# Optimization experiments

Measured on AMD Instinct MI355X. Metric: run time of the kernel, lower is better.

Reference implementation:

```python
import jax, jax.numpy as jnp
import numpy as np

B, H, E, R, T = 2048, 512, 300, 512, 50


def setup_inputs() -> dict:
    key = jax.random.key(0)
    ks = jax.random.split(key, 12)
    s = 0.02  # xavier-ish scale for params
    return {
        "x": jax.random.normal(ks[0], (B, E), jnp.float32),
        "h_enc": jax.random.normal(ks[1], (B, R), jnp.float32),
        "phi_history": jax.random.normal(ks[2], (T, B, H), jnp.float32),
        "cell_history": jax.random.normal(ks[3], (T, B, H), jnp.float32),
        "h_summ": jax.random.normal(ks[4], (B, H), jnp.float32),
        "c_summ": jax.random.normal(ks[5], (B, H), jnp.float32),
        "W_w": jax.random.normal(ks[6], (4 * H, H + E), jnp.float32) * s,
        "W_b": jnp.zeros((4 * H,), jnp.float32),
        "v_w": jax.random.normal(ks[7], (1, H), jnp.float32) * s,
        "v_b": jnp.zeros((1,), jnp.float32),
        "lq_w": jax.random.normal(ks[8], (H, R), jnp.float32) * s,
        "lq_b": jnp.zeros((H,), jnp.float32),
        "lk_w": jax.random.normal(ks[9], (H, H), jnp.float32) * s,
        "lk_b": jnp.zeros((H,), jnp.float32),
        "ls_w": jax.random.normal(ks[10], (H, H), jnp.float32) * s,
        "ls_b": jnp.zeros((H,), jnp.float32),
    }


def reference(x, h_enc, phi_history, cell_history, h_summ, c_summ,
              W_w, W_b, v_w, v_b, lq_w, lq_b, lk_w, lk_b, ls_w, ls_b):
    Hd = h_summ.shape[-1]
    # [T,B,H] -> [B,T,H] (torch.stack(...).transpose(0,1))
    phi = jnp.transpose(phi_history, (1, 0, 2))
    cell = jnp.transpose(cell_history, (1, 0, 2))
    # additive attention over cached history
    q = h_enc @ lq_w.T + lq_b                       # [B,H]
    k = jnp.einsum('bth,ah->bta', phi, lk_w) + lk_b  # [B,T,H]
    su = h_summ @ ls_w.T + ls_b                     # [B,H]
    e = jnp.tanh(q[:, None, :] + k + su[:, None, :])
    scores = jnp.einsum('bth,oh->bto', e, v_w)[..., 0] + v_b[0]  # [B,T]
    p = jax.nn.softmax(scores, axis=-1)
    h_s = jnp.einsum('bt,bth->bh', p, phi)
    c_s = jnp.einsum('bt,bth->bh', p, cell)
    # fused LSTM gates on [h_summ, x]
    gates = jnp.concatenate([h_s, x], axis=1) @ W_w.T + W_b  # [B,4H]
    f_t = jax.nn.sigmoid(gates[:, :Hd])
    o_t = jax.nn.sigmoid(gates[:, Hd:2 * Hd])
    i_t = jax.nn.sigmoid(gates[:, 2 * Hd:3 * Hd])
    ch_t = jnp.tanh(gates[:, 3 * Hd:])
    c_ctrl = f_t * c_s + i_t * ch_t
    h_ctrl = o_t * jnp.tanh(c_ctrl)
    return h_ctrl
```

## Files before the change

### kernel.cpp

```cpp
#include <hip/hip_runtime.h>
#include <math.h>

#define Bm 2048
#define Hm 512
#define Em 300
#define Tm 50
#define KWm 812
#define KWp 832

typedef unsigned short u16;
typedef unsigned int u32;
typedef __attribute__((ext_vector_type(8))) short short8;
typedef __attribute__((ext_vector_type(8))) u16 ushort8v;
typedef __attribute__((ext_vector_type(4))) float f32x4;

__device__ __forceinline__ float sigmoidf_(float x) { return 1.f / (1.f + __expf(-x)); }

__device__ __forceinline__ u16 bfr(float x) {
    union { float f; u32 u; } c; c.f = x;
    u32 u = c.u;
    u += 0x7FFFu + ((u >> 16) & 1u);
    return (u16)(u >> 16);
}
__device__ __forceinline__ ushort8v cvt8(const float* __restrict__ p) {
    f32x4 v0 = *(const f32x4*)p;
    f32x4 v1 = *(const f32x4*)(p + 4);
    ushort8v r;
    r[0] = bfr(v0[0]); r[1] = bfr(v0[1]); r[2] = bfr(v0[2]); r[3] = bfr(v0[3]);
    r[4] = bfr(v1[0]); r[5] = bfr(v1[1]); r[6] = bfr(v1[2]); r[7] = bfr(v1[3]);
    return r;
}

__device__ __forceinline__ void gload16(const u16* g, u16* l) {
    __builtin_amdgcn_global_load_lds((const __attribute__((address_space(1))) void*)g,
                                     (__attribute__((address_space(3))) void*)l, 16, 0, 0);
}

__global__ __launch_bounds__(256) void k_pack_phi(
        const float* __restrict__ phi, u16* __restrict__ phib) {
    const size_t nvec = (size_t)Tm * Bm * 512 / 8;
    for (size_t i = (size_t)blockIdx.x * 256 + threadIdx.x; i < nvec;
         i += (size_t)gridDim.x * 256)
        *(ushort8v*)&phib[i * 8] = cvt8(phi + i * 8);
}

__global__ __launch_bounds__(256) void k_pack(
        const float* __restrict__ henc, const float* __restrict__ hsum,
        const float* __restrict__ lq, const float* __restrict__ ls,
        const float* __restrict__ Ww, const float* __restrict__ x,
        const float* __restrict__ lkw,
        u16* __restrict__ Aq, u16* __restrict__ Wq,
        u16* __restrict__ Wg, u16* __restrict__ Xb, u16* __restrict__ lkwb) {
    const int job = blockIdx.y;
    const int r = blockIdx.x;
    const int tid = threadIdx.x;
    if (job == 0) {
        for (int c = tid; c < 1024; c += 256) {
            float v = (c < 512) ? henc[(size_t)r * 512 + c] : hsum[(size_t)r * 512 + (c - 512)];
            Aq[(size_t)r * 1024 + c] = bfr(v);
        }
    } else if (job == 1) {
        if (r < 512)
            for (int c = tid; c < 1024; c += 256) {
                float v = (c < 512) ? lq[(size_t)r * 512 + c] : ls[(size_t)r * 512 + (c - 512)];
                Wq[(size_t)r * 1024 + c] = bfr(v);
            }
    } else if (job == 2) {
        for (int c = tid; c < KWp; c += 256)
            Wg[(size_t)r * KWp + c] = (c < KWm) ? bfr(Ww[(size_t)r * KWm + c]) : (u16)0;
    } else if (job == 3) {
        for (int c = 512 + tid; c < KWp; c += 256)
            Xb[(size_t)r * KWp + c] = (c < KWm) ? bfr(x[(size_t)r * Em + (c - 512)]) : (u16)0;
    } else {
        if (r < 512)
            for (int c = tid; c < 512; c += 256)
                lkwb[(size_t)r * 512 + c] = bfr(lkw[(size_t)r * 512 + c]);
    }
}

__global__ __launch_bounds__(256) void k_qs_mfma(
        const u16* __restrict__ Aq, const u16* __restrict__ Wq,
        const float* __restrict__ lqb, const float* __restrict__ lsb,
        const float* __restrict__ lkb, float* __restrict__ qs) {
    __shared__ u16 Asl[64 * 32];
    __shared__ u16 Bsl[64 * 32];
    const int m0 = blockIdx.x * 64, n0 = blockIdx.y * 64;
    const int tid = threadIdx.x, lane = tid & 63, wid = tid >> 6;
    const int wr = wid >> 1, wc = wid & 1;
    const int l15 = lane & 15, l4 = lane >> 4;
    const int srow = (wid << 4) + (lane >> 2);
    const int gchunk = (lane & 3) ^ ((srow >> 1) & 3);
    f32x4 acc[2][2];
    #pragma unroll
    for (int i = 0; i < 2; ++i)
        #pragma unroll
        for (int j = 0; j < 2; ++j) acc[i][j] = (f32x4){0.f, 0.f, 0.f, 0.f};

    for (int k0 = 0; k0 < 1024; k0 += 32) {
        __syncthreads();
        gload16(Aq + (size_t)(m0 + srow) * 1024 + k0 + gchunk * 8, &Asl[wid * 512]);
        gload16(Wq + (size_t)(n0 + srow) * 1024 + k0 + gchunk * 8, &Bsl[wid * 512]);
        __syncthreads();
        short8 af[2], bf[2];
        #pragma unroll
        for (int mf = 0; mf < 2; ++mf) {
            int r = wr * 32 + mf * 16 + l15;
            af[mf] = *(const short8*)&Asl[r * 32 + (l4 ^ ((r >> 1) & 3)) * 8];
        }
        #pragma unroll
        for (int nf = 0; nf < 2; ++nf) {
            int r = wc * 32 + nf * 16 + l15;
            bf[nf] = *(const short8*)&Bsl[r * 32 + (l4 ^ ((r >> 1) & 3)) * 8];
        }
        #pragma unroll
        for (int mf = 0; mf < 2; ++mf)
            #pragma unroll
            for (int nf = 0; nf < 2; ++nf)
                acc[mf][nf] = __builtin_amdgcn_mfma_f32_16x16x32_bf16(
                                  af[mf], bf[nf], acc[mf][nf], 0, 0, 0);
    }
    #pragma unroll
    for (int mf = 0; mf < 2; ++mf)
        #pragma unroll
        for (int nf = 0; nf < 2; ++nf)
            #pragma unroll
            for (int reg = 0; reg < 4; ++reg) {
                int b = m0 + wr * 32 + mf * 16 + l4 * 4 + reg;
                int h = n0 + wc * 32 + nf * 16 + l15;
                qs[(size_t)b * Hm + h] = acc[mf][nf][reg] + lqb[h] + lsb[h] + lkb[h];
            }
}

__global__ __launch_bounds__(256) void k_scores_mfma(
        const u16* __restrict__ phib, const u16* __restrict__ lkwb,
        const float* __restrict__ qs2, const float* __restrict__ vw,
        float* __restrict__ scores) {
    __shared__ u16 Asl[128 * 32];
    __shared__ u16 Bsl[128 * 32];
    const int n0 = blockIdx.x * 128;
    const int m0 = blockIdx.y * 128;
    const int t  = m0 >> 11;
    const int b0 = m0 & (Bm - 1);
    const int tid = threadIdx.x, lane = tid & 63, wid = tid >> 6;
    const int wr = wid >> 1, wc = wid & 1;
    const int l15 = lane & 15, l4 = lane >> 4;
    const int srow_base = (wid << 5) + (lane >> 2);
    const int schunk = lane & 3;

    f32x4 acc[4][4];
    #pragma unroll
    for (int i = 0; i < 4; ++i)
        #pragma unroll
        for (int j = 0; j < 4; ++j) acc[i][j] = (f32x4){0.f, 0.f, 0.f, 0.f};

    for (int k0 = 0; k0 < 512; k0 += 32) {
        __syncthreads();
        #pragma unroll
        for (int j = 0; j < 2; ++j) {
            int r = srow_base + j * 16;
            int gc = schunk ^ ((r >> 1) & 3);
            gload16(phib + (size_t)(m0 + r) * 512 + k0 + gc * 8,
                    &Asl[((wid << 5) + j * 16) * 32]);
            gload16(lkwb + (size_t)(n0 + r) * 512 + k0 + gc * 8,
                    &Bsl[((wid << 5) + j * 16) * 32]);
        }
        __syncthreads();
        short8 af[4], bf[4];
        #pragma unroll
        for (int mf = 0; mf < 4; ++mf) {
            int r = wr * 64 + mf * 16 + l15;
            af[mf] = *(const short8*)&Asl[r * 32 + (l4 ^ ((r >> 1) & 3)) * 8];
        }
        #pragma unroll
        for (int nf = 0; nf < 4; ++nf) {
            int r = wc * 64 + nf * 16 + l15;
            bf[nf] = *(const short8*)&Bsl[r * 32 + (l4 ^ ((r >> 1) & 3)) * 8];
        }
        #pragma unroll
        for (int mf = 0; mf < 4; ++mf)
            #pragma unroll
            for (int nf = 0; nf < 4; ++nf)
                acc[mf][nf] = __builtin_amdgcn_mfma_f32_16x16x32_bf16(
                                  af[mf], bf[nf], acc[mf][nf], 0, 0, 0);
    }

    float vws[4];
    int av[4];
    #pragma unroll
    for (int nf = 0; nf < 4; ++nf) {
        av[nf] = n0 + wc * 64 + nf * 16 + l15;
        vws[nf] = vw[av[nf]];
    }
    #pragma unroll
    for (int mf = 0; mf < 4; ++mf) {
        #pragma unroll
        for (int reg = 0; reg < 4; ++reg) {
            int b = b0 + wr * 64 + mf * 16 + l4 * 4 + reg;
            const float* q = qs2 + (size_t)b * Hm;
            float s = 0.f;
            #pragma unroll
            for (int nf = 0; nf < 4; ++nf)
                s = fmaf(tanhf(acc[mf][nf][reg] + q[av[nf]]), vws[nf], s);
            #pragma unroll
            for (int o = 1; o < 16; o <<= 1) s += __shfl_xor(s, o);
            if (l15 == 0) atomicAdd(&scores[(size_t)b * Tm + t], s);
        }
    }
}

__global__ __launch_bounds__(256) void k_attn(
        const u16* __restrict__ phib, const float* __restrict__ cell,
        const float* __restrict__ scores,
        u16* __restrict__ Xb, float* __restrict__ cs) {
    __shared__ float p[Tm];
    const int b = blockIdx.x;
    const int tid = threadIdx.x;
    if (tid < 64) {
        float s = (tid < Tm) ? scores[(size_t)b * Tm + tid] : -INFINITY;
        float m = s;
        #pragma unroll
        for (int o = 32; o; o >>= 1) m = fmaxf(m, __shfl_xor(m, o));
        float ex = (tid < Tm) ? __expf(s - m) : 0.f;
        float sum = ex;
        #pragma unroll
        for (int o = 32; o; o >>= 1) sum += __shfl_xor(sum, o);
        if (tid < Tm) p[tid] = ex / sum;
    }
    __syncthreads();
    const int c0 = tid * 2;
    float ah0 = 0.f, ah1 = 0.f, ac0 = 0.f, ac1 = 0.f;
    for (int t = 0; t < Tm; ++t) {
        float w = p[t];
        const size_t rb = ((size_t)t * Bm + b) * 512 + c0;
        u32 ph2 = *(const u32*)&phib[rb];
        float2 ce2 = *(const float2*)&cell[rb];
        float p0 = __uint_as_float(ph2 << 16);
        float p1 = __uint_as_float(ph2 & 0xFFFF0000u);
        ah0 = fmaf(w, p0, ah0);
        ah1 = fmaf(w, p1, ah1);
        ac0 = fmaf(w, ce2.x, ac0);
        ac1 = fmaf(w, ce2.y, ac1);
    }
    *(u32*)&Xb[(size_t)b * KWp + c0] = (u32)bfr(ah0) | ((u32)bfr(ah1) << 16);
    *(float2*)&cs[(size_t)b * Hm + c0] = make_float2(ac0, ac1);
}

__global__ __launch_bounds__(256) void k_gates_mfma(
        const u16* __restrict__ Xb, const u16* __restrict__ Wg,
        float* __restrict__ gates) {
    __shared__ u16 Asl[64 * 32];
    __shared__ u16 Bsl[128 * 32];
    const int m0 = blockIdx.x * 64, n0 = blockIdx.y * 128;
    const int tid = threadIdx.x, lane = tid & 63, wid = tid >> 6;
    const int wr = wid >> 1, wc = wid & 1;
    const int l15 = lane & 15, l4 = lane >> 4;
    const int srow = (wid << 4) + (lane >> 2);
    const int gchunkA = (lane & 3) ^ ((srow >> 1) & 3);
    f32x4 acc[2][4];
    #pragma unroll
    for (int i = 0; i < 2; ++i)
        #pragma unroll
        for (int j = 0; j < 4; ++j) acc[i][j] = (f32x4){0.f, 0.f, 0.f, 0.f};

    for (int k0 = 0; k0 < KWp; k0 += 32) {
        __syncthreads();
        gload16(Xb + (size_t)(m0 + srow) * KWp + k0 + gchunkA * 8, &Asl[wid * 512]);
        #pragma unroll
        for (int j = 0; j < 2; ++j) {
            int brow = (wid << 5) + (j << 4) + (lane >> 2);
            int gchunkB = (lane & 3) ^ ((brow >> 1) & 3);
            gload16(Wg + (size_t)(n0 + brow) * KWp + k0 + gchunkB * 8,
                    &Bsl[wid * 1024 + j * 512]);
        }
        __syncthreads();
        short8 af[2], bf[4];
        #pragma unroll
        for (int mf = 0; mf < 2; ++mf) {
            int r = wr * 32 + mf * 16 + l15;
            af[mf] = *(const short8*)&Asl[r * 32 + (l4 ^ ((r >> 1) & 3)) * 8];
        }
        #pragma unroll
        for (int nf = 0; nf < 4; ++nf) {
            int r = wc * 64 + nf * 16 + l15;
            bf[nf] = *(const short8*)&Bsl[r * 32 + (l4 ^ ((r >> 1) & 3)) * 8];
        }
        #pragma unroll
        for (int mf = 0; mf < 2; ++mf)
            #pragma unroll
            for (int nf = 0; nf < 4; ++nf)
                acc[mf][nf] = __builtin_amdgcn_mfma_f32_16x16x32_bf16(
                                  af[mf], bf[nf], acc[mf][nf], 0, 0, 0);
    }
    #pragma unroll
    for (int mf = 0; mf < 2; ++mf)
        #pragma unroll
        for (int nf = 0; nf < 4; ++nf)
            #pragma unroll
            for (int reg = 0; reg < 4; ++reg) {
                int b = m0 + wr * 32 + mf * 16 + l4 * 4 + reg;
                int n = n0 + wc * 64 + nf * 16 + l15;
                gates[(size_t)b * 2048 + n] = acc[mf][nf][reg];
            }
}

__global__ __launch_bounds__(256) void k_lstm(
        const float* __restrict__ gates, const float* __restrict__ Wb,
        const float* __restrict__ cs, float* __restrict__ out) {
    const int idx = blockIdx.x * 256 + threadIdx.x;
    const int b = idx >> 9, h = idx & 511;
    const float* g = gates + (size_t)b * 2048;
    float f  = sigmoidf_(g[h]        + Wb[h]);
    float o  = sigmoidf_(g[512 + h]  + Wb[512 + h]);
    float ii = sigmoidf_(g[1024 + h] + Wb[1024 + h]);
    float ch = tanhf(    g[1536 + h] + Wb[1536 + h]);
    float c  = f * cs[idx] + ii * ch;
    out[idx] = o * tanhf(c);
}

extern "C" void kernel_launch(void* const* d_in, const int* in_sizes, int n_in,
                              void* d_out, int out_size, void* d_ws, size_t ws_size,
                              hipStream_t stream) {
    const float* x      = (const float*)d_in[0];
    const float* h_enc  = (const float*)d_in[1];
    const float* phi    = (const float*)d_in[2];
    const float* cell   = (const float*)d_in[3];
    const float* h_summ = (const float*)d_in[4];
    const float* W_w    = (const float*)d_in[6];
    const float* W_b    = (const float*)d_in[7];
    const float* v_w    = (const float*)d_in[8];
    const float* lq_w   = (const float*)d_in[10];
    const float* lq_b   = (const float*)d_in[11];
    const float* lk_w   = (const float*)d_in[12];
    const float* lk_b   = (const float*)d_in[13];
    const float* ls_w   = (const float*)d_in[14];
    const float* ls_b   = (const float*)d_in[15];
    float* out = (float*)d_out;

    char* w = (char*)d_ws;
    u16*   phib   = (u16*)  (w);
    float* gates  = (float*)(w);
    float* qs     = (float*)(w + 104857600);
    float* scores = (float*)(w + 109051904);
    float* cs     = (float*)(w + 109461504);
    u16*   Aq     = (u16*)  (w + 113655808);
    u16*   Wq     = (u16*)  (w + 117850112);
    u16*   Wg     = (u16*)  (w + 118898688);
    u16*   Xb     = (u16*)  (w + 122306560);
    u16*   lkwb   = (u16*)  (w + 125714432);

    hipMemsetAsync(scores, 0, (size_t)Bm * Tm * sizeof(float), stream);
    k_pack<<<dim3(2048, 5), 256, 0, stream>>>(h_enc, h_summ, lq_w, ls_w, W_w, x, lk_w,
                                              Aq, Wq, Wg, Xb, lkwb);
    k_pack_phi<<<dim3(2048), 256, 0, stream>>>(phi, phib);
    k_qs_mfma<<<dim3(Bm / 64, Hm / 64), 256, 0, stream>>>(Aq, Wq, lq_b, ls_b, lk_b, qs);
    k_scores_mfma<<<dim3(Hm / 128, (Tm * Bm) / 128), 256, 0, stream>>>(phib, lkwb, qs, v_w, scores);
    k_attn<<<dim3(Bm), 256, 0, stream>>>(phib, cell, scores, Xb, cs);
    k_gates_mfma<<<dim3(Bm / 64, 2048 / 128), 256, 0, stream>>>(Xb, Wg, gates);
    k_lstm<<<dim3((Bm * Hm) / 256), 256, 0, stream>>>(gates, W_b, cs, out);
}
```

Before: 340.8 us.

## Double-buffer LDS tiles in scores MFMA kernel to overlap loads with compute

Splits the shared-memory A/B tiles of the attention-score GEMM into two buffers. Each iteration prefetches the next K-slice while running MFMAs on the current one, using an explicit vmcnt wait and raw barriers instead of two __syncthreads per step. The aim is to hide global-to-LDS latency behind matrix work. It doubles LDS use to 32 KB per block, which may reduce occupancy, and it relies on a hand-counted vmcnt value being correct.

```diff
diff --git a/kernel.cpp b/kernel.cpp
--- a/kernel.cpp
+++ b/kernel.cpp
@@ -135,8 +135,8 @@
         const u16* __restrict__ phib, const u16* __restrict__ lkwb,
         const float* __restrict__ qs2, const float* __restrict__ vw,
         float* __restrict__ scores) {
-    __shared__ u16 Asl[128 * 32];
-    __shared__ u16 Bsl[128 * 32];
+    __shared__ u16 Asl[2][128 * 32];
+    __shared__ u16 Bsl[2][128 * 32];
     const int n0 = blockIdx.x * 128;
     const int m0 = blockIdx.y * 128;
     const int t  = m0 >> 11;
@@ -153,28 +153,28 @@
         #pragma unroll
         for (int j = 0; j < 4; ++j) acc[i][j] = (f32x4){0.f, 0.f, 0.f, 0.f};
 
-    for (int k0 = 0; k0 < 512; k0 += 32) {
-        __syncthreads();
+    auto STAGE = [&](int buf, int k0) {
         #pragma unroll
         for (int j = 0; j < 2; ++j) {
             int r = srow_base + j * 16;
             int gc = schunk ^ ((r >> 1) & 3);
             gload16(phib + (size_t)(m0 + r) * 512 + k0 + gc * 8,
-                    &Asl[((wid << 5) + j * 16) * 32]);
+                    &Asl[buf][((wid << 5) + j * 16) * 32]);
             gload16(lkwb + (size_t)(n0 + r) * 512 + k0 + gc * 8,
-                    &Bsl[((wid << 5) + j * 16) * 32]);
-        }
-        __syncthreads();
+                    &Bsl[buf][((wid << 5) + j * 16) * 32]);
+        }
+    };
+    auto COMPUTE = [&](int buf) {
         short8 af[4], bf[4];
         #pragma unroll
         for (int mf = 0; mf < 4; ++mf) {
             int r = wr * 64 + mf * 16 + l15;
-            af[mf] = *(const short8*)&Asl[r * 32 + (l4 ^ ((r >> 1) & 3)) * 8];
+            af[mf] = *(const short8*)&Asl[buf][r * 32 + (l4 ^ ((r >> 1) & 3)) * 8];
         }
         #pragma unroll
         for (int nf = 0; nf < 4; ++nf) {
             int r = wc * 64 + nf * 16 + l15;
-            bf[nf] = *(const short8*)&Bsl[r * 32 + (l4 ^ ((r >> 1) & 3)) * 8];
+            bf[nf] = *(const short8*)&Bsl[buf][r * 32 + (l4 ^ ((r >> 1) & 3)) * 8];
         }
         #pragma unroll
         for (int mf = 0; mf < 4; ++mf)
@@ -182,7 +182,23 @@
             for (int nf = 0; nf < 4; ++nf)
                 acc[mf][nf] = __builtin_amdgcn_mfma_f32_16x16x32_bf16(
                                   af[mf], bf[nf], acc[mf][nf], 0, 0, 0);
-    }
+    };
+
+    STAGE(0, 0);
+    int cur = 0;
+    #pragma unroll 1
+    for (int kt = 0; kt < 15; ++kt) {
+        STAGE(cur ^ 1, (kt + 1) << 5);
+        asm volatile("s_waitcnt vmcnt(4)" ::: "memory");
+        __builtin_amdgcn_s_barrier();
+        COMPUTE(cur);
+        __builtin_amdgcn_sched_barrier(0);
+        __builtin_amdgcn_s_barrier();
+        cur ^= 1;
+    }
+    asm volatile("s_waitcnt vmcnt(0)" ::: "memory");
+    __builtin_amdgcn_s_barrier();
+    COMPUTE(cur);
 
     float vws[4];
     int av[4];
```

After: 345.7 us. About the same (+1.4%).

## Deepen scores GEMM K-tile to 64, remap blocks for XCD locality, fast tanh

Applied to the files above, without the earlier changes.

The scores GEMM now stages a 64-wide K slice per iteration with an XOR swizzle over 8 chunks. This halves the number of barrier pairs and doubles the MFMA work per sync. The 1-D grid is remapped so consecutive blocks on each of the 8 XCDs share M tiles, which should improve L2 reuse of phi. MFMA issue is wrapped in s_setprio. tanhf is replaced by an exp-based fast tanh in the score epilogue and the LSTM, which costs some accuracy and may overflow to inf for large inputs (though the formula still saturates to 1 correctly).

```diff
diff --git a/kernel.cpp b/kernel.cpp
--- a/kernel.cpp
+++ b/kernel.cpp
@@ -15,6 +15,7 @@
 typedef __attribute__((ext_vector_type(4))) float f32x4;
 
 __device__ __forceinline__ float sigmoidf_(float x) { return 1.f / (1.f + __expf(-x)); }
+__device__ __forceinline__ float tanhfast(float x) { return 1.f - 2.f / (__expf(2.f * x) + 1.f); }
 
 __device__ __forceinline__ u16 bfr(float x) {
     union { float f; u32 u; } c; c.f = x;
@@ -135,17 +136,19 @@
         const u16* __restrict__ phib, const u16* __restrict__ lkwb,
         const float* __restrict__ qs2, const float* __restrict__ vw,
         float* __restrict__ scores) {
-    __shared__ u16 Asl[128 * 32];
-    __shared__ u16 Bsl[128 * 32];
-    const int n0 = blockIdx.x * 128;
-    const int m0 = blockIdx.y * 128;
+    __shared__ u16 Asl[128 * 64];
+    __shared__ u16 Bsl[128 * 64];
+    const int d  = blockIdx.x;
+    const int wg = (d & 7) * 400 + (d >> 3);
+    const int n0 = (wg & 3) << 7;
+    const int m0 = (wg >> 2) << 7;
     const int t  = m0 >> 11;
     const int b0 = m0 & (Bm - 1);
     const int tid = threadIdx.x, lane = tid & 63, wid = tid >> 6;
     const int wr = wid >> 1, wc = wid & 1;
     const int l15 = lane & 15, l4 = lane >> 4;
-    const int srow_base = (wid << 5) + (lane >> 2);
-    const int schunk = lane & 3;
+    const int srow_in = lane >> 3;
+    const int schunk  = (lane & 7) ^ srow_in;
 
     f32x4 acc[4][4];
     #pragma unroll
@@ -153,35 +156,47 @@
         #pragma unroll
         for (int j = 0; j < 4; ++j) acc[i][j] = (f32x4){0.f, 0.f, 0.f, 0.f};
 
-    for (int k0 = 0; k0 < 512; k0 += 32) {
-        __syncthreads();
-        #pragma unroll
-        for (int j = 0; j < 2; ++j) {
-            int r = srow_base + j * 16;
-            int gc = schunk ^ ((r >> 1) & 3);
-            gload16(phib + (size_t)(m0 + r) * 512 + k0 + gc * 8,
-                    &Asl[((wid << 5) + j * 16) * 32]);
-            gload16(lkwb + (size_t)(n0 + r) * 512 + k0 + gc * 8,
-                    &Bsl[((wid << 5) + j * 16) * 32]);
-        }
-        __syncthreads();
-        short8 af[4], bf[4];
+    for (int kt = 0; kt < 8; ++kt) {
+        const int k0 = kt << 6;
+        __syncthreads();
+        #pragma unroll
+        for (int j = 0; j < 4; ++j) {
+            int r = (wid << 5) + (j << 3) + srow_in;
+            gload16(phib + (size_t)(m0 + r) * 512 + k0 + schunk * 8,
+                    &Asl[((wid << 5) + (j << 3)) * 64]);
+            gload16(lkwb + (size_t)(n0 + r) * 512 + k0 + schunk * 8,
+                    &Bsl[((wid << 5) + (j << 3)) * 64]);
+        }
+        __syncthreads();
+        short8 af[4][2], bf[4][2];
         #pragma unroll
         for (int mf = 0; mf < 4; ++mf) {
             int r = wr * 64 + mf * 16 + l15;
-            af[mf] = *(const short8*)&Asl[r * 32 + (l4 ^ ((r >> 1) & 3)) * 8];
+            #pragma unroll
+            for (int ks = 0; ks < 2; ++ks) {
+                int c = ks * 4 + l4;
+                af[mf][ks] = *(const short8*)&Asl[r * 64 + (c ^ (r & 7)) * 8];
+            }
         }
         #pragma unroll
         for (int nf = 0; nf < 4; ++nf) {
             int r = wc * 64 + nf * 16 + l15;
-            bf[nf] = *(const short8*)&Bsl[r * 32 + (l4 ^ ((r >> 1) & 3)) * 8];
-        }
-        #pragma unroll
-        for (int mf = 0; mf < 4; ++mf)
-            #pragma unroll
-            for (int nf = 0; nf < 4; ++nf)
-                acc[mf][nf] = __builtin_amdgcn_mfma_f32_16x16x32_bf16(
-                                  af[mf], bf[nf], acc[mf][nf], 0, 0, 0);
+            #pragma unroll
+            for (int ks = 0; ks < 2; ++ks) {
+                int c = ks * 4 + l4;
+                bf[nf][ks] = *(const short8*)&Bsl[r * 64 + (c ^ (r & 7)) * 8];
+            }
+        }
+        __builtin_amdgcn_s_setprio(1);
+        #pragma unroll
+        for (int ks = 0; ks < 2; ++ks)
+            #pragma unroll
+            for (int mf = 0; mf < 4; ++mf)
+                #pragma unroll
+                for (int nf = 0; nf < 4; ++nf)
+                    acc[mf][nf] = __builtin_amdgcn_mfma_f32_16x16x32_bf16(
+                                      af[mf][ks], bf[nf][ks], acc[mf][nf], 0, 0, 0);
+        __builtin_amdgcn_s_setprio(0);
     }
 
     float vws[4];
@@ -200,7 +215,7 @@
             float s = 0.f;
             #pragma unroll
             for (int nf = 0; nf < 4; ++nf)
-                s = fmaf(tanhf(acc[mf][nf][reg] + q[av[nf]]), vws[nf], s);
+                s = fmaf(tanhfast(acc[mf][nf][reg] + q[av[nf]]), vws[nf], s);
             #pragma unroll
             for (int o = 1; o < 16; o <<= 1) s += __shfl_xor(s, o);
             if (l15 == 0) atomicAdd(&scores[(size_t)b * Tm + t], s);
@@ -312,9 +327,9 @@
     float f  = sigmoidf_(g[h]        + Wb[h]);
     float o  = sigmoidf_(g[512 + h]  + Wb[512 + h]);
     float ii = sigmoidf_(g[1024 + h] + Wb[1024 + h]);
-    float ch = tanhf(    g[1536 + h] + Wb[1536 + h]);
+    float ch = tanhfast( g[1536 + h] + Wb[1536 + h]);
     float c  = f * cs[idx] + ii * ch;
-    out[idx] = o * tanhf(c);
+    out[idx] = o * tanhfast(c);
 }
 
 extern "C" void kernel_launch(void* const* d_in, const int* in_sizes, int n_in,
@@ -353,7 +368,7 @@
                                               Aq, Wq, Wg, Xb, lkwb);
     k_pack_phi<<<dim3(2048), 256, 0, stream>>>(phi, phib);
     k_qs_mfma<<<dim3(Bm / 64, Hm / 64), 256, 0, stream>>>(Aq, Wq, lq_b, ls_b, lk_b, qs);
-    k_scores_mfma<<<dim3(Hm / 128, (Tm * Bm) / 128), 256, 0, stream>>>(phib, lkwb, qs, v_w, scores);
+    k_scores_mfma<<<dim3(3200), 256, 0, stream>>>(phib, lkwb, qs, v_w, scores);
     k_attn<<<dim3(Bm), 256, 0, stream>>>(phib, cell, scores, Xb, cs);
     k_gates_mfma<<<dim3(Bm / 64, 2048 / 128), 256, 0, stream>>>(Xb, Wg, gates);
     k_lstm<<<dim3((Bm * Hm) / 256), 256, 0, stream>>>(gates, W_b, cs, out);
```

Measured after the change: 310.5 us. 8.9% less time.

## Restructure scores GEMM to full-K phi tiles with per-block score reduction

Applied to the files above, without the earlier changes.

The scores kernel now gives each block 64 rows of phi with the full 512-wide K dimension staged once in LDS (swizzled). Each of the four waves covers 128 output columns and reads the lk_w fragments straight from global/L2 instead of through LDS. The per-column partial scores are reduced in shared memory and written once, which removes the global atomics and the scores memset. A cheaper exp-based tanh replaces tanhf in the scores epilogue and the LSTM kernel. The trade-offs are 64KB of LDS per block, which limits occupancy, higher register pressure from 32 accumulators, and repeated global reads of the weight matrix.

```diff
diff --git a/kernel.cpp b/kernel.cpp
--- a/kernel.cpp
+++ b/kernel.cpp
@@ -15,6 +15,7 @@
 typedef __attribute__((ext_vector_type(4))) float f32x4;
 
 __device__ __forceinline__ float sigmoidf_(float x) { return 1.f / (1.f + __expf(-x)); }
+__device__ __forceinline__ float tanhfast(float x) { return 1.f - 2.f / (__expf(2.f * x) + 1.f); }
 
 __device__ __forceinline__ u16 bfr(float x) {
     union { float f; u32 u; } c; c.f = x;
@@ -131,81 +132,85 @@
             }
 }
 
-__global__ __launch_bounds__(256) void k_scores_mfma(
+__global__ __launch_bounds__(256, 2) void k_scores_mfma(
         const u16* __restrict__ phib, const u16* __restrict__ lkwb,
         const float* __restrict__ qs2, const float* __restrict__ vw,
         float* __restrict__ scores) {
-    __shared__ u16 Asl[128 * 32];
-    __shared__ u16 Bsl[128 * 32];
-    const int n0 = blockIdx.x * 128;
-    const int m0 = blockIdx.y * 128;
+    __shared__ u16 Asl[64 * 512];
+    __shared__ float sred[4][64];
+    const int m0 = blockIdx.x * 64;
     const int t  = m0 >> 11;
     const int b0 = m0 & (Bm - 1);
     const int tid = threadIdx.x, lane = tid & 63, wid = tid >> 6;
-    const int wr = wid >> 1, wc = wid & 1;
     const int l15 = lane & 15, l4 = lane >> 4;
-    const int srow_base = (wid << 5) + (lane >> 2);
-    const int schunk = lane & 3;
-
-    f32x4 acc[4][4];
+    const int n0 = wid << 7;
+
+    #pragma unroll
+    for (int j = 0; j < 16; ++j) {
+        int row = wid * 16 + j;
+        gload16(phib + (size_t)(m0 + row) * 512 + ((lane ^ (row & 7)) << 3),
+                &Asl[row * 512]);
+    }
+    __syncthreads();
+
+    int ae[4], ao[4];
+    #pragma unroll
+    for (int mf = 0; mf < 4; ++mf) {
+        int r = mf * 16 + l15;
+        int x = r & 7;
+        int base = r * 512 + ((l4 ^ (x & 3)) << 3);
+        ae[mf] = base + ((x & 4) ? 32 : 0);
+        ao[mf] = base + ((x & 4) ? 0 : 32);
+    }
+    const u16* bpp[8];
+    #pragma unroll
+    for (int nf = 0; nf < 8; ++nf)
+        bpp[nf] = lkwb + (size_t)(n0 + nf * 16 + l15) * 512 + l4 * 8;
+
+    f32x4 acc[4][8];
     #pragma unroll
     for (int i = 0; i < 4; ++i)
         #pragma unroll
-        for (int j = 0; j < 4; ++j) acc[i][j] = (f32x4){0.f, 0.f, 0.f, 0.f};
-
-    for (int k0 = 0; k0 < 512; k0 += 32) {
-        __syncthreads();
-        #pragma unroll
-        for (int j = 0; j < 2; ++j) {
-            int r = srow_base + j * 16;
-            int gc = schunk ^ ((r >> 1) & 3);
-            gload16(phib + (size_t)(m0 + r) * 512 + k0 + gc * 8,
-                    &Asl[((wid << 5) + j * 16) * 32]);
-            gload16(lkwb + (size_t)(n0 + r) * 512 + k0 + gc * 8,
-                    &Bsl[((wid << 5) + j * 16) * 32]);
-        }
-        __syncthreads();
-        short8 af[4], bf[4];
-        #pragma unroll
-        for (int mf = 0; mf < 4; ++mf) {
-            int r = wr * 64 + mf * 16 + l15;
-            af[mf] = *(const short8*)&Asl[r * 32 + (l4 ^ ((r >> 1) & 3)) * 8];
-        }
-        #pragma unroll
-        for (int nf = 0; nf < 4; ++nf) {
-            int r = wc * 64 + nf * 16 + l15;
-            bf[nf] = *(const short8*)&Bsl[r * 32 + (l4 ^ ((r >> 1) & 3)) * 8];
-        }
+        for (int j = 0; j < 8; ++j) acc[i][j] = (f32x4){0.f, 0.f, 0.f, 0.f};
+
+    #pragma unroll
+    for (int ks = 0; ks < 16; ++ks) {
+        short8 af[4], bf[8];
+        #pragma unroll
+        for (int nf = 0; nf < 8; ++nf)
+            bf[nf] = *(const short8*)&bpp[nf][ks * 32];
         #pragma unroll
         for (int mf = 0; mf < 4; ++mf)
-            #pragma unroll
-            for (int nf = 0; nf < 4; ++nf)
+            af[mf] = *(const short8*)&Asl[((ks & 1) ? ao[mf] : ae[mf]) + (ks >> 1) * 64];
+        #pragma unroll
+        for (int mf = 0; mf < 4; ++mf)
+            #pragma unroll
+            for (int nf = 0; nf < 8; ++nf)
                 acc[mf][nf] = __builtin_amdgcn_mfma_f32_16x16x32_bf16(
                                   af[mf], bf[nf], acc[mf][nf], 0, 0, 0);
     }
 
-    float vws[4];
-    int av[4];
-    #pragma unroll
-    for (int nf = 0; nf < 4; ++nf) {
-        av[nf] = n0 + wc * 64 + nf * 16 + l15;
-        vws[nf] = vw[av[nf]];
-    }
     #pragma unroll
     for (int mf = 0; mf < 4; ++mf) {
         #pragma unroll
         for (int reg = 0; reg < 4; ++reg) {
-            int b = b0 + wr * 64 + mf * 16 + l4 * 4 + reg;
-            const float* q = qs2 + (size_t)b * Hm;
+            int row = mf * 16 + l4 * 4 + reg;
+            const float* q = qs2 + (size_t)(b0 + row) * Hm;
             float s = 0.f;
             #pragma unroll
-            for (int nf = 0; nf < 4; ++nf)
-                s = fmaf(tanhf(acc[mf][nf][reg] + q[av[nf]]), vws[nf], s);
+            for (int nf = 0; nf < 8; ++nf) {
+                int col = n0 + nf * 16 + l15;
+                s = fmaf(tanhfast(acc[mf][nf][reg] + q[col]), vw[col], s);
+            }
             #pragma unroll
             for (int o = 1; o < 16; o <<= 1) s += __shfl_xor(s, o);
-            if (l15 == 0) atomicAdd(&scores[(size_t)b * Tm + t], s);
-        }
-    }
+            if (l15 == 0) sred[wid][row] = s;
+        }
+    }
+    __syncthreads();
+    if (tid < 64)
+        scores[(size_t)(b0 + tid) * Tm + t] =
+            sred[0][tid] + sred[1][tid] + sred[2][tid] + sred[3][tid];
 }
 
 __global__ __launch_bounds__(256) void k_attn(
@@ -312,9 +317,9 @@
     float f  = sigmoidf_(g[h]        + Wb[h]);
     float o  = sigmoidf_(g[512 + h]  + Wb[512 + h]);
     float ii = sigmoidf_(g[1024 + h] + Wb[1024 + h]);
-    float ch = tanhf(    g[1536 + h] + Wb[1536 + h]);
+    float ch = tanhfast( g[1536 + h] + Wb[1536 + h]);
     float c  = f * cs[idx] + ii * ch;
-    out[idx] = o * tanhf(c);
+    out[idx] = o * tanhfast(c);
 }
 
 extern "C" void kernel_launch(void* const* d_in, const int* in_sizes, int n_in,
@@ -348,12 +353,11 @@
     u16*   Xb     = (u16*)  (w + 122306560);
     u16*   lkwb   = (u16*)  (w + 125714432);
 
-    hipMemsetAsync(scores, 0, (size_t)Bm * Tm * sizeof(float), stream);
     k_pack<<<dim3(2048, 5), 256, 0, stream>>>(h_enc, h_summ, lq_w, ls_w, W_w, x, lk_w,
                                               Aq, Wq, Wg, Xb, lkwb);
     k_pack_phi<<<dim3(2048), 256, 0, stream>>>(phi, phib);
     k_qs_mfma<<<dim3(Bm / 64, Hm / 64), 256, 0, stream>>>(Aq, Wq, lq_b, ls_b, lk_b, qs);
-    k_scores_mfma<<<dim3(Hm / 128, (Tm * Bm) / 128), 256, 0, stream>>>(phib, lkwb, qs, v_w, scores);
+    k_scores_mfma<<<dim3((Tm * Bm) / 64), 256, 0, stream>>>(phib, lkwb, qs, v_w, scores);
     k_attn<<<dim3(Bm), 256, 0, stream>>>(phib, cell, scores, Xb, cs);
     k_gates_mfma<<<dim3(Bm / 64, 2048 / 128), 256, 0, stream>>>(Xb, Wg, gates);
     k_lstm<<<dim3((Bm * Hm) / 256), 256, 0, stream>>>(gates, W_b, cs, out);
```

Measured after the change: 327.4 us. 1.04x faster.
